# Kernel tuning notes

Hardware: AMD Instinct MI355X
Metric: run time of the kernel (lower is better)

Reference implementation:

```python
import jax, jax.numpy as jnp
import numpy as np
import math

M = 4096   # mem_dim == hidden_size (required: C @ qt)
D = 2048   # input_size


def setup_inputs() -> dict:
    key = jax.random.key(0)
    ks = jax.random.split(key, 16)
    f = lambda k, s: jax.random.normal(k, s, dtype=jnp.float32)
    return {
        "x": f(ks[0], (D, 1)),
        "cp": f(ks[1], (M, M)),
        "n_prev": f(ks[2], (M, 1)),
        "Wq": f(ks[3], (M, D)),
        "bq": f(ks[4], (M, 1)),
        "Wk": f(ks[5], (M, D)),
        "bk": f(ks[6], (M, 1)),
        "Wv": f(ks[7], (M, D)),
        "bV": f(ks[8], (M, 1)),
        "Wi": f(ks[9], (1, D)),
        "bi": f(ks[10], (1,)),
        "Wf": f(ks[11], (1, D)),
        "bf": f(ks[12], (1,)),
        "Wo": f(ks[13], (1, D)),
        "bo": f(ks[14], (1,)),
    }


def reference(x, cp, n_prev, Wq, bq, Wk, bk, Wv, bV, Wi, bi, Wf, bf, Wo, bo):
    inv_sqrt_m = 1.0 / math.sqrt(M)
    qt = Wq @ x + bq                      # (M, 1)
    kt = inv_sqrt_m * (Wk @ x + bk)       # (M, 1)
    vt = Wv @ x + bV                      # (M, 1)
    it = jnp.exp(Wi @ x + bi)             # (1, 1) input gate (exp)
    ft = jnp.exp(Wf @ x + bf)             # (1, 1) forget gate (exp)
    v = vt[:, 0]                          # (M,)
    k = kt[:, 0]                          # (M,)
    # matrix memory update: C = f*C_prev + i * v k^T
    C = ft * cp + it * jnp.outer(v, k)    # (M, M)
    n = ft * n_prev + it * k[:, None]     # (M, 1)
    denom = jnp.maximum(jnp.abs(n.T @ qt), 1.0)   # (1, 1)
    h_tilde = (C @ qt) / denom            # (M, 1)
    ot = jax.nn.sigmoid(Wo @ x + bo)      # (1, 1)
    ht = ot * h_tilde                     # (M, 1)
    return (ht, C, n)
```

## Files before the change

### kernel.cpp

```cpp
#include <hip/hip_runtime.h>
#include <math.h>

#define MM 4096
#define DD 2048

typedef float floatx4 __attribute__((ext_vector_type(4)));


__global__ __launch_bounds__(256) void k1_gemv_gates(
    const float* __restrict__ x,
    const float* __restrict__ Wq, const float* __restrict__ bq,
    const float* __restrict__ Wk, const float* __restrict__ bk,
    const float* __restrict__ Wv, const float* __restrict__ bV,
    const float* __restrict__ Wi, const float* __restrict__ bi,
    const float* __restrict__ Wf, const float* __restrict__ bf,
    const float* __restrict__ Wo, const float* __restrict__ bo,
    float* __restrict__ ws)
{
    const int lane = threadIdx.x & 63;
    const int wid  = threadIdx.x >> 6;

    if (blockIdx.x >= 3072) {
        __shared__ double gred[4];
        const int g = blockIdx.x - 3072;
        const float* G = (g == 0) ? Wi : ((g == 1) ? Wf : Wo);
        const float4* g4 = (const float4*)G;
        const float4* xv = (const float4*)x;
        double acc = 0.0;
        for (int t = threadIdx.x; t < DD / 4; t += 256) {
            float4 gg = g4[t];
            float4 xx = xv[t];
            acc += (double)gg.x * xx.x + (double)gg.y * xx.y
                 + (double)gg.z * xx.z + (double)gg.w * xx.w;
        }
        for (int off = 32; off; off >>= 1) acc += __shfl_down(acc, off, 64);
        if (lane == 0) gred[wid] = acc;
        __syncthreads();
        if (threadIdx.x == 0) {
            double s = gred[0] + gred[1] + gred[2] + gred[3];
            if (g == 0)      ws[3 * MM + 0] = (float)exp(s + (double)bi[0]);
            else if (g == 1) ws[3 * MM + 1] = (float)exp(s + (double)bf[0]);
            else             ws[3 * MM + 2] = (float)(1.0 / (1.0 + exp(-(s + (double)bo[0]))));
        }
        return;
    }

    __shared__ float xs[DD];

    {
        const float4* xv  = (const float4*)x;
        float4*       xsv = (float4*)xs;
        xsv[threadIdx.x]       = xv[threadIdx.x];
        xsv[256 + threadIdx.x] = xv[256 + threadIdx.x];
    }
    __syncthreads();

    const int m   = blockIdx.x >> 10;
    const int row = ((blockIdx.x & 1023) << 2) + wid;

    const float* W = (m == 0) ? Wq : ((m == 1) ? Wk : Wv);
    const float4* w4  = (const float4*)(W + (size_t)row * DD);
    const float4* xs4 = (const float4*)xs;

    float acc = 0.f;
    #pragma unroll
    for (int t = 0; t < DD / 4 / 64; ++t) {
        float4 ww = w4 [t * 64 + lane];
        float4 xx = xs4[t * 64 + lane];
        acc += ww.x * xx.x + ww.y * xx.y + ww.z * xx.z + ww.w * xx.w;
    }

    for (int off = 32; off; off >>= 1) acc += __shfl_down(acc, off, 64);

    if (lane == 0) {
        if (m == 0)      ws[row]          = acc + bq[row];
        else if (m == 1) ws[MM + row]     = (acc + bk[row]) * (1.0f / 64.0f);
        else             ws[2 * MM + row] = acc + bV[row];
    }
}

__global__ __launch_bounds__(256) void k2_rowC(
    const float* __restrict__ cp, const float* __restrict__ n_prev,
    float* __restrict__ ws, float* __restrict__ C_out, float* __restrict__ n_out)
{
    const int lane = threadIdx.x & 63;
    const int wid  = threadIdx.x >> 6;

    if (blockIdx.x == MM) {
        __shared__ float pred[4];
        const float it = ws[3 * MM + 0];
        const float ft = ws[3 * MM + 1];
        const float4* np4 = (const float4*)n_prev;
        const float4* kv4 = (const float4*)(ws + MM);
        const float4* qv4 = (const float4*)ws;
        float4* n4 = (float4*)n_out;
        float acc = 0.f;
        #pragma unroll
        for (int u = 0; u < 4; ++u) {
            int t = threadIdx.x + 256 * u;
            float4 np = np4[t], kk = kv4[t], qq = qv4[t];
            float4 nn;
            nn.x = fmaf(ft, np.x, it * kk.x);
            nn.y = fmaf(ft, np.y, it * kk.y);
            nn.z = fmaf(ft, np.z, it * kk.z);
            nn.w = fmaf(ft, np.w, it * kk.w);
            n4[t] = nn;
            acc += nn.x * qq.x + nn.y * qq.y + nn.z * qq.z + nn.w * qq.w;
        }
        for (int off = 32; off; off >>= 1) acc += __shfl_down(acc, off, 64);
        if (lane == 0) pred[wid] = acc;
        __syncthreads();
        if (threadIdx.x == 0) {
            float s = pred[0] + pred[1] + pred[2] + pred[3];
            ws[3 * MM + 3] = fmaxf(fabsf(s), 1.0f);
        }
        return;
    }

    __shared__ float sred[4];
    const int row = blockIdx.x;
    const float it  = ws[3 * MM + 0];
    const float ft  = ws[3 * MM + 1];
    const float ivi = it * ws[2 * MM + row];

    const float4* cprow = (const float4*)(cp + (size_t)row * MM);
    const float4* kv4   = (const float4*)(ws + MM);
    const float4* qv4   = (const float4*)ws;
    float4*       crow  = (float4*)(C_out + (size_t)row * MM);

    float4 c[4], kk[4], qq[4];
    #pragma unroll
    for (int u = 0; u < 4; ++u) c[u]  = cprow[threadIdx.x + 256 * u];
    #pragma unroll
    for (int u = 0; u < 4; ++u) kk[u] = kv4[threadIdx.x + 256 * u];
    #pragma unroll
    for (int u = 0; u < 4; ++u) qq[u] = qv4[threadIdx.x + 256 * u];

    float acc = 0.f;
    #pragma unroll
    for (int u = 0; u < 4; ++u) {
        float4 o;
        o.x = fmaf(ivi, kk[u].x, ft * c[u].x);
        o.y = fmaf(ivi, kk[u].y, ft * c[u].y);
        o.z = fmaf(ivi, kk[u].z, ft * c[u].z);
        o.w = fmaf(ivi, kk[u].w, ft * c[u].w);
        crow[threadIdx.x + 256 * u] = o;
        acc += o.x * qq[u].x + o.y * qq[u].y + o.z * qq[u].z + o.w * qq[u].w;
    }
    for (int off = 32; off; off >>= 1) acc += __shfl_down(acc, off, 64);
    if (lane == 0) sred[wid] = acc;
    __syncthreads();
    if (threadIdx.x == 0)
        ws[4 * MM + row] = sred[0] + sred[1] + sred[2] + sred[3];
}

__global__ __launch_bounds__(256) void k3_finalize(
    const float* __restrict__ ws, float* __restrict__ ht_out)
{
    const float ot    = ws[3 * MM + 2];
    const float denom = ws[3 * MM + 3];
    const int i = blockIdx.x * 256 + threadIdx.x;
    ht_out[i] = ot * (ws[4 * MM + i] / denom);
}

extern "C" void kernel_launch(void* const* d_in, const int* in_sizes, int n_in,
                              void* d_out, int out_size, void* d_ws, size_t ws_size,
                              hipStream_t stream)
{
    const float* x      = (const float*)d_in[0];
    const float* cp     = (const float*)d_in[1];
    const float* n_prev = (const float*)d_in[2];
    const float* Wq = (const float*)d_in[3];
    const float* bq = (const float*)d_in[4];
    const float* Wk = (const float*)d_in[5];
    const float* bk = (const float*)d_in[6];
    const float* Wv = (const float*)d_in[7];
    const float* bV = (const float*)d_in[8];
    const float* Wi = (const float*)d_in[9];
    const float* bi = (const float*)d_in[10];
    const float* Wf = (const float*)d_in[11];
    const float* bf = (const float*)d_in[12];
    const float* Wo = (const float*)d_in[13];
    const float* bo = (const float*)d_in[14];

    float* out = (float*)d_out;
    float* ht  = out;
    float* C   = out + MM;
    float* n   = out + MM + (size_t)MM * MM;
    float* ws  = (float*)d_ws;

    k1_gemv_gates<<<3075, 256, 0, stream>>>(x, Wq, bq, Wk, bk, Wv, bV,
                                            Wi, bi, Wf, bf, Wo, bo, ws);
    k2_rowC      <<<MM + 1, 256, 0, stream>>>(cp, n_prev, ws, C, n);
    k3_finalize  <<<MM / 256, 256, 0, stream>>>(ws, ht);
}
```

Measured before the change: 222.1 us.

## Fuse GEMV, gates, memory update and readout into one cooperative kernel

Replaces the three-kernel pipeline with a single cooperative kernel of 1024 blocks. Each block computes q/k/v for four rows plus the scalar gates redundantly, writes partial denominators, and then does one grid-wide sync. After the sync the same block updates four rows of C and computes h directly, so the separate finalize kernel and the extra launches go away. The costs are redundant gate work in every block and a grid barrier, which only runs correctly if all 1024 blocks can be resident at once. If the cooperative launch fails, the code falls back to the old kernels.

```diff
diff --git a/kernel.cpp b/kernel.cpp
--- a/kernel.cpp
+++ b/kernel.cpp
@@ -1,13 +1,164 @@
 #include <hip/hip_runtime.h>
+#include <hip/hip_cooperative_groups.h>
 #include <math.h>
 
 #define MM 4096
 #define DD 2048
-
-typedef float floatx4 __attribute__((ext_vector_type(4)));
-
-
-__global__ __launch_bounds__(256) void k1_gemv_gates(
+#define DEN_BASE 8192
+
+namespace cg = cooperative_groups;
+
+__device__ __forceinline__ float aload(const float* p)
+{
+    return __hip_atomic_load(p, __ATOMIC_RELAXED, __HIP_MEMORY_SCOPE_AGENT);
+}
+
+__global__ __launch_bounds__(256, 4) void fused(
+    const float* __restrict__ x,  const float* __restrict__ cp,
+    const float* __restrict__ n_prev,
+    const float* __restrict__ Wq, const float* __restrict__ bq,
+    const float* __restrict__ Wk, const float* __restrict__ bk,
+    const float* __restrict__ Wv, const float* __restrict__ bV,
+    const float* __restrict__ Wi, const float* __restrict__ bi,
+    const float* __restrict__ Wf, const float* __restrict__ bf,
+    const float* __restrict__ Wo, const float* __restrict__ bo,
+    float* __restrict__ ws, float* __restrict__ ht,
+    float* __restrict__ C_out, float* __restrict__ n_out)
+{
+    cg::grid_group grid = cg::this_grid();
+    const int tid  = threadIdx.x;
+    const int lane = tid & 63;
+    const int wid  = tid >> 6;
+    const int b    = blockIdx.x;
+
+    __shared__ float xs[DD];
+    __shared__ float gates[3];
+    __shared__ float vloc[4];
+    __shared__ float dred[4];
+    __shared__ float dsr[4];
+    __shared__ float sred[4];
+
+    {
+        const float4* xv  = (const float4*)x;
+        float4*       xsv = (float4*)xs;
+        xsv[tid]       = xv[tid];
+        xsv[256 + tid] = xv[256 + tid];
+    }
+    __syncthreads();
+
+    const float4* xs4 = (const float4*)xs;
+
+    if (wid < 3) {
+        const float* G = (wid == 0) ? Wi : ((wid == 1) ? Wf : Wo);
+        const float4* g4 = (const float4*)G;
+        double acc = 0.0;
+        #pragma unroll
+        for (int t = 0; t < 8; ++t) {
+            float4 gg = g4[t * 64 + lane], xx = xs4[t * 64 + lane];
+            acc += (double)gg.x * xx.x + (double)gg.y * xx.y
+                 + (double)gg.z * xx.z + (double)gg.w * xx.w;
+        }
+        for (int off = 32; off; off >>= 1) acc += __shfl_down(acc, off, 64);
+        if (lane == 0) {
+            if (wid == 0)      gates[0] = (float)exp(acc + (double)bi[0]);
+            else if (wid == 1) gates[1] = (float)exp(acc + (double)bf[0]);
+            else               gates[2] = (float)(1.0 / (1.0 + exp(-(acc + (double)bo[0]))));
+        }
+    }
+
+    const int row = b * 4 + wid;
+    float aq = 0.f, ak = 0.f, av = 0.f;
+    {
+        const float4* q4 = (const float4*)(Wq + (size_t)row * DD);
+        const float4* k4 = (const float4*)(Wk + (size_t)row * DD);
+        const float4* v4 = (const float4*)(Wv + (size_t)row * DD);
+        #pragma unroll
+        for (int t = 0; t < 8; ++t) {
+            float4 xx = xs4[t * 64 + lane];
+            float4 qq = q4[t * 64 + lane];
+            float4 kk = k4[t * 64 + lane];
+            float4 vv = v4[t * 64 + lane];
+            aq += qq.x * xx.x + qq.y * xx.y + qq.z * xx.z + qq.w * xx.w;
+            ak += kk.x * xx.x + kk.y * xx.y + kk.z * xx.z + kk.w * xx.w;
+            av += vv.x * xx.x + vv.y * xx.y + vv.z * xx.z + vv.w * xx.w;
+        }
+        for (int off = 32; off; off >>= 1) {
+            aq += __shfl_down(aq, off, 64);
+            ak += __shfl_down(ak, off, 64);
+            av += __shfl_down(av, off, 64);
+        }
+    }
+    __syncthreads();
+
+    if (lane == 0) {
+        const float it = gates[0], ft = gates[1];
+        const float qt = aq + bq[row];
+        const float kk = (ak + bk[row]) * (1.0f / 64.0f);
+        const float vv = av + bV[row];
+        ws[row]      = qt;
+        ws[MM + row] = kk;
+        vloc[wid]    = vv;
+        const float nr = fmaf(ft, n_prev[row], it * kk);
+        n_out[row]   = nr;
+        dred[wid]    = nr * qt;
+    }
+    __syncthreads();
+    if (tid == 0)
+        ws[DEN_BASE + 32 * b] = dred[0] + dred[1] + dred[2] + dred[3];
+
+    __threadfence();
+    grid.sync();
+    __threadfence();
+
+    const float it = gates[0], ft = gates[1], ot = gates[2];
+
+    float dsum = 0.f;
+    #pragma unroll
+    for (int u = 0; u < 4; ++u)
+        dsum += aload(ws + DEN_BASE + 32 * (tid + 256 * u));
+    for (int off = 32; off; off >>= 1) dsum += __shfl_down(dsum, off, 64);
+    if (lane == 0) dsr[wid] = dsum;
+    __syncthreads();
+    const float denom = fmaxf(fabsf(dsr[0] + dsr[1] + dsr[2] + dsr[3]), 1.0f);
+
+    float kkv[16], qqv[16];
+    #pragma unroll
+    for (int u = 0; u < 4; ++u) {
+        const int base = 4 * (tid + 256 * u);
+        #pragma unroll
+        for (int e = 0; e < 4; ++e) {
+            kkv[4 * u + e] = aload(ws + MM + base + e);
+            qqv[4 * u + e] = aload(ws + base + e);
+        }
+    }
+
+    for (int j = 0; j < 4; ++j) {
+        const int r = b * 4 + j;
+        const float ivi = it * vloc[j];
+        const float4* cprow = (const float4*)(cp + (size_t)r * MM);
+        float4*       crow  = (float4*)(C_out + (size_t)r * MM);
+        float acc = 0.f;
+        #pragma unroll
+        for (int u = 0; u < 4; ++u) {
+            float4 c = cprow[tid + 256 * u];
+            float4 o;
+            o.x = fmaf(ivi, kkv[4 * u + 0], ft * c.x);
+            o.y = fmaf(ivi, kkv[4 * u + 1], ft * c.y);
+            o.z = fmaf(ivi, kkv[4 * u + 2], ft * c.z);
+            o.w = fmaf(ivi, kkv[4 * u + 3], ft * c.w);
+            crow[tid + 256 * u] = o;
+            acc += o.x * qqv[4 * u + 0] + o.y * qqv[4 * u + 1]
+                 + o.z * qqv[4 * u + 2] + o.w * qqv[4 * u + 3];
+        }
+        for (int off = 32; off; off >>= 1) acc += __shfl_down(acc, off, 64);
+        if (lane == 0) sred[wid] = acc;
+        __syncthreads();
+        if (tid == 0) ht[r] = ot * ((sred[0] + sred[1] + sred[2] + sred[3]) / denom);
+        __syncthreads();
+    }
+}
+
+__global__ __launch_bounds__(256, 4) void k1_gemv_gates(
     const float* __restrict__ x,
     const float* __restrict__ Wq, const float* __restrict__ bq,
     const float* __restrict__ Wk, const float* __restrict__ bk,
@@ -46,7 +197,6 @@
     }
 
     __shared__ float xs[DD];
-
     {
         const float4* xv  = (const float4*)x;
         float4*       xsv = (float4*)xs;
@@ -64,12 +214,11 @@
 
     float acc = 0.f;
     #pragma unroll
-    for (int t = 0; t < DD / 4 / 64; ++t) {
+    for (int t = 0; t < 8; ++t) {
         float4 ww = w4 [t * 64 + lane];
         float4 xx = xs4[t * 64 + lane];
         acc += ww.x * xx.x + ww.y * xx.y + ww.z * xx.z + ww.w * xx.w;
     }
-
     for (int off = 32; off; off >>= 1) acc += __shfl_down(acc, off, 64);
 
     if (lane == 0) {
@@ -189,8 +338,18 @@
     float* n   = out + MM + (size_t)MM * MM;
     float* ws  = (float*)d_ws;
 
-    k1_gemv_gates<<<3075, 256, 0, stream>>>(x, Wq, bq, Wk, bk, Wv, bV,
-                                            Wi, bi, Wf, bf, Wo, bo, ws);
-    k2_rowC      <<<MM + 1, 256, 0, stream>>>(cp, n_prev, ws, C, n);
-    k3_finalize  <<<MM / 256, 256, 0, stream>>>(ws, ht);
-}
+    void* args[] = {
+        (void*)&x, (void*)&cp, (void*)&n_prev,
+        (void*)&Wq, (void*)&bq, (void*)&Wk, (void*)&bk, (void*)&Wv, (void*)&bV,
+        (void*)&Wi, (void*)&bi, (void*)&Wf, (void*)&bf, (void*)&Wo, (void*)&bo,
+        (void*)&ws, (void*)&ht, (void*)&C, (void*)&n
+    };
+    hipError_t err = hipLaunchCooperativeKernel((const void*)fused, dim3(1024),
+                                                dim3(256), args, 0, stream);
+    if (err != hipSuccess) {
+        k1_gemv_gates<<<3075, 256, 0, stream>>>(x, Wq, bq, Wk, bk, Wv, bV,
+                                                Wi, bi, Wf, bf, Wo, bo, ws);
+        k2_rowC      <<<MM + 1, 256, 0, stream>>>(cp, n_prev, ws, C, n);
+        k3_finalize  <<<MM / 256, 256, 0, stream>>>(ws, ht);
+    }
+}
```

Measured after the change: 508.4 us. 2.29x slower.
